# Performance work log

Hardware: AMD Instinct MI355X
Metric: run time of the kernel (lower is better)

The kernel has to match this reference:

```python
import jax, jax.numpy as jnp
import numpy as np

NUCLEIC_ACID_CUTOFF = 30.0
OTHER_CUTOFF = 15.0


def _cdist(x):
    # x: [b, n, 3] -> pairwise euclidean distances [b, n, n]
    sq = jnp.sum(x * x, axis=-1)  # [b, n]
    d2 = sq[:, :, None] + sq[:, None, :] - 2.0 * jnp.einsum('bid,bjd->bij', x, x)
    d2 = jnp.maximum(d2, 0.0)
    # safe sqrt (zero diagonal would produce nan grads otherwise)
    safe = jnp.where(d2 > 0.0, d2, 1.0)
    return jnp.where(d2 > 0.0, jnp.sqrt(safe), 0.0)


def setup_inputs() -> dict:
    key = jax.random.key(0)
    k1, k2, k3, k4, k5 = jax.random.split(key, 5)
    b, n = 2, 4096
    # scale ~10 Angstrom spread so distances straddle the 15/30 cutoffs
    true_coords = jax.random.normal(k1, (b, n, 3), dtype=jnp.float32) * 10.0
    pred_coords = true_coords + jax.random.normal(k2, (b, n, 3), dtype=jnp.float32) * 1.5
    is_dna = jax.random.bernoulli(k3, 0.15, (b, n))
    is_rna = jax.random.bernoulli(k4, 0.15, (b, n))
    coords_mask = jax.random.bernoulli(k5, 0.95, (b, n))
    return {
        'pred_coords': pred_coords,
        'true_coords': true_coords,
        'is_dna': is_dna,
        'is_rna': is_rna,
        'coords_mask': coords_mask,
    }


def reference(pred_coords, true_coords, is_dna, is_rna, coords_mask):
    n = pred_coords.shape[1]
    pred_dists = _cdist(pred_coords)  # [b, n, n]
    true_dists = _cdist(true_coords)  # [b, n, n]
    dist_diff = jnp.abs(true_dists - pred_dists)
    eps = (
        jax.nn.sigmoid(0.5 - dist_diff)
        + jax.nn.sigmoid(1.0 - dist_diff)
        + jax.nn.sigmoid(2.0 - dist_diff)
        + jax.nn.sigmoid(4.0 - dist_diff)
    ) / 4.0

    is_nucleotide = is_dna | is_rna  # [b, n]
    is_nucleotide_pair = is_nucleotide[:, :, None] & is_nucleotide[:, None, :]
    inclusion_radius = jnp.where(
        is_nucleotide_pair,
        true_dists < NUCLEIC_ACID_CUTOFF,
        true_dists < OTHER_CUTOFF,
    )
    not_eye = ~jnp.eye(n, dtype=bool)[None, :, :]
    mask = inclusion_radius & not_eye
    mask = mask & (coords_mask[:, :, None] & coords_mask[:, None, :])

    maskf = mask.astype(eps.dtype)
    lddt_sum = jnp.sum(eps * maskf, axis=(-1, -2))  # [b]
    lddt_count = jnp.sum(maskf, axis=(-1, -2))  # [b]
    lddt = lddt_sum / jnp.maximum(lddt_count, 1.0)
    return 1.0 - jnp.mean(lddt)
```

## Files before the change

### kernel.cpp

```cpp
#include <hip/hip_runtime.h>
#include <hip/hip_bf16.h>


#define NRES 4096
#define NBATCH 2
#define TI 8

#define CUT15 21.6404256133f
#define CUT30 43.2808512267f

#define S1 66.35420923f
#define S2 678.60880385f
#define S3 2039.58217570f
#define S4 1808.04241445f
#define QP1 16.58855231f
#define QP2 339.30440193f
#define QP3 1529.68663177f
#define QP4 1808.04241445f

#define DIAG_EPS 0.80408219445f
#define LOG2E 1.44269504089f

__global__ void pack_kernel(const float* __restrict__ pred,
                            const float* __restrict__ truec,
                            const int* __restrict__ dna,
                            const int* __restrict__ rna,
                            const int* __restrict__ cm,
                            float4* __restrict__ tp,
                            float4* __restrict__ pp,
                            float* __restrict__ acc)
{
    int idx = blockIdx.x * 256 + threadIdx.x;
    if (idx >= NRES * NBATCH) return;
    float nuc = ((dna[idx] | rna[idx]) != 0) ? 1.0f : 0.0f;
    float cmf = (cm[idx] != 0) ? 1.0f : 0.0f;
    tp[idx] = make_float4(truec[3*idx+0]*LOG2E, truec[3*idx+1]*LOG2E, truec[3*idx+2]*LOG2E, nuc);
    pp[idx] = make_float4(pred[3*idx+0]*LOG2E,  pred[3*idx+1]*LOG2E,  pred[3*idx+2]*LOG2E,  cmf);

    float v = cmf;
    #pragma unroll
    for (int o = 32; o > 0; o >>= 1) v += __shfl_down(v, o, 64);
    if ((threadIdx.x & 63) == 0) atomicAdd(&acc[4 + (idx >> 12)], v);
}

__launch_bounds__(256, 4)
__global__ void lddt_main(const float4* __restrict__ tp,
                          const float4* __restrict__ pp,
                          float* __restrict__ acc)
{
    const int b    = blockIdx.y;
    const int i0   = blockIdx.x * TI;
    const int base = b * NRES;
    const int tid  = threadIdx.x;

    float tix[TI], tiy[TI], tiz[TI];
    float pix[TI], piy[TI], piz[TI];
    float cHi[TI], cLo[TI];
    #pragma unroll
    for (int r = 0; r < TI; ++r) {
        float4 t4 = tp[base + i0 + r];
        float4 p4 = pp[base + i0 + r];
        tix[r] = t4.x; tiy[r] = t4.y; tiz[r] = t4.z;
        pix[r] = p4.x; piy[r] = p4.y; piz[r] = p4.z;
        bool cmi  = (p4.w != 0.0f);
        bool nuci = (t4.w != 0.0f);
        cHi[r] = cmi ? (nuci ? CUT30 : CUT15) : -1.0f;
        cLo[r] = cmi ? CUT15 : -1.0f;
    }

    float s = 0.0f, c = 0.0f;

    float4 t4 = tp[base + tid];
    float4 p4 = pp[base + tid];

    #pragma unroll 1
    for (int jt = 0; jt < NRES / 256; ++jt) {
        const int jn = tid + (((jt + 1) & 15) << 8);
        float4 t4n = tp[base + jn];
        float4 p4n = pp[base + jn];

        const float wj   = p4.w;
        const bool  nucj = (t4.w != 0.0f);

        #pragma unroll
        for (int r = 0; r < TI; ++r) {
            float dx = tix[r] - t4.x, dy = tiy[r] - t4.y, dz = tiz[r] - t4.z;
            float dt = __builtin_amdgcn_sqrtf(dx*dx + dy*dy + dz*dz);
            float ex = pix[r] - p4.x, ey = piy[r] - p4.y, ez = piz[r] - p4.z;
            float dp = __builtin_amdgcn_sqrtf(ex*ex + ey*ey + ez*ez);

            float cutoff = nucj ? cHi[r] : cLo[r];
            float mf = (dt < cutoff) ? wj : 0.0f;

            float t = __builtin_amdgcn_exp2f(-fabsf(dt - dp));
            float Q  = 1.0f + t*(S1 + t*(S2 + t*(S3 + t*S4)));
            float Qp = QP1 + t*(QP2 + t*(QP3 + t*QP4));
            float rq = __builtin_amdgcn_rcpf(Q);

            s += mf * ((t * Qp) * rq);
            c += mf;
        }

        t4 = t4n; p4 = p4n;
    }

    #pragma unroll
    for (int o = 32; o > 0; o >>= 1) {
        s += __shfl_down(s, o, 64);
        c += __shfl_down(c, o, 64);
    }

    __shared__ float red_s[4];
    __shared__ float red_c[4];
    const int wid  = tid >> 6;
    const int lane = tid & 63;
    if (lane == 0) { red_s[wid] = s; red_c[wid] = c; }
    __syncthreads();

    if (tid == 0) {
        float ts = red_s[0] + red_s[1] + red_s[2] + red_s[3];
        float tc = red_c[0] + red_c[1] + red_c[2] + red_c[3];
        atomicAdd(&acc[b], ts);
        atomicAdd(&acc[NBATCH + b], tc);
    }
}

__global__ void lddt_final(const float* __restrict__ acc, float* __restrict__ out)
{
    float M0 = acc[4], M1 = acc[5];
    float l0 = (acc[0] - DIAG_EPS * M0) / fmaxf(acc[2] - M0, 1.0f);
    float l1 = (acc[1] - DIAG_EPS * M1) / fmaxf(acc[3] - M1, 1.0f);
    out[0] = 1.0f - 0.5f * (l0 + l1);
}

extern "C" void kernel_launch(void* const* d_in, const int* in_sizes, int n_in,
                              void* d_out, int out_size, void* d_ws, size_t ws_size,
                              hipStream_t stream) {
    const float* pred  = (const float*)d_in[0];
    const float* truec = (const float*)d_in[1];
    const int*   dna   = (const int*)d_in[2];
    const int*   rna   = (const int*)d_in[3];
    const int*   cmask = (const int*)d_in[4];
    float* out = (float*)d_out;

    char* ws = (char*)d_ws;
    float*  acc = (float*)ws;
    float4* tp  = (float4*)(ws + 1024);
    float4* pp  = (float4*)(ws + 1024 + NBATCH*NRES*16);

    (void)hipMemsetAsync(acc, 0, 8 * sizeof(float), stream);

    pack_kernel<<<(NRES*NBATCH + 255)/256, 256, 0, stream>>>(pred, truec, dna, rna, cmask, tp, pp, acc);

    dim3 grid(NRES / TI, NBATCH);
    lddt_main<<<grid, 256, 0, stream>>>(tp, pp, acc);

    lddt_final<<<1, 1, 0, stream>>>(acc, out);
}
```

Measured before the change: 54.90 us.

## Exploit pair symmetry to compute only the upper triangle of residue pairs

Splits the j dimension into 1024-wide tiles and launches a 3D grid. Blocks whose j-tile lies entirely at or below the i rows exit immediately, and straddling tiles mask out j<=i with an index compare. Because distances, cutoffs and masks are symmetric, summing only j>i halves both the numerator and the count, so the ratio is unchanged. This also removes the diagonal correction and the coords-mask count reduction. In exchange, the hot loop gains an extra compare per pair, and the grid launches many blocks that return without doing work.

```diff
diff --git a/kernel.cpp b/kernel.cpp
--- a/kernel.cpp
+++ b/kernel.cpp
@@ -5,6 +5,7 @@
 #define NRES 4096
 #define NBATCH 2
 #define TI 8
+#define JTILE 1024
 
 #define CUT15 21.6404256133f
 #define CUT30 43.2808512267f
@@ -18,7 +19,6 @@
 #define QP3 1529.68663177f
 #define QP4 1808.04241445f
 
-#define DIAG_EPS 0.80408219445f
 #define LOG2E 1.44269504089f
 
 __global__ void pack_kernel(const float* __restrict__ pred,
@@ -27,8 +27,7 @@
                             const int* __restrict__ rna,
                             const int* __restrict__ cm,
                             float4* __restrict__ tp,
-                            float4* __restrict__ pp,
-                            float* __restrict__ acc)
+                            float4* __restrict__ pp)
 {
     int idx = blockIdx.x * 256 + threadIdx.x;
     if (idx >= NRES * NBATCH) return;
@@ -36,11 +35,6 @@
     float cmf = (cm[idx] != 0) ? 1.0f : 0.0f;
     tp[idx] = make_float4(truec[3*idx+0]*LOG2E, truec[3*idx+1]*LOG2E, truec[3*idx+2]*LOG2E, nuc);
     pp[idx] = make_float4(pred[3*idx+0]*LOG2E,  pred[3*idx+1]*LOG2E,  pred[3*idx+2]*LOG2E,  cmf);
-
-    float v = cmf;
-    #pragma unroll
-    for (int o = 32; o > 0; o >>= 1) v += __shfl_down(v, o, 64);
-    if ((threadIdx.x & 63) == 0) atomicAdd(&acc[4 + (idx >> 12)], v);
 }
 
 __launch_bounds__(256, 4)
@@ -48,14 +42,20 @@
                           const float4* __restrict__ pp,
                           float* __restrict__ acc)
 {
-    const int b    = blockIdx.y;
-    const int i0   = blockIdx.x * TI;
+    const int b     = blockIdx.z;
+    const int jt    = blockIdx.y;
+    const int i0    = blockIdx.x * TI;
+    const int jbase = jt * JTILE;
+
+    if (jbase + JTILE - 1 <= i0) return;
+
     const int base = b * NRES;
     const int tid  = threadIdx.x;
+    const bool straddle = (i0 >> 10) == jt;
 
     float tix[TI], tiy[TI], tiz[TI];
     float pix[TI], piy[TI], piz[TI];
-    float cHi[TI], cLo[TI];
+    float cHi[TI], cLo[TI], jminf[TI];
     #pragma unroll
     for (int r = 0; r < TI; ++r) {
         float4 t4 = tp[base + i0 + r];
@@ -66,21 +66,23 @@
         bool nuci = (t4.w != 0.0f);
         cHi[r] = cmi ? (nuci ? CUT30 : CUT15) : -1.0f;
         cLo[r] = cmi ? CUT15 : -1.0f;
+        jminf[r] = straddle ? (float)(i0 + r) + 0.5f : -1.0f;
     }
 
     float s = 0.0f, c = 0.0f;
 
-    float4 t4 = tp[base + tid];
-    float4 p4 = pp[base + tid];
+    float4 t4 = tp[base + jbase + tid];
+    float4 p4 = pp[base + jbase + tid];
 
     #pragma unroll 1
-    for (int jt = 0; jt < NRES / 256; ++jt) {
-        const int jn = tid + (((jt + 1) & 15) << 8);
+    for (int jtl = 0; jtl < JTILE / 256; ++jtl) {
+        const int jn = jbase + tid + (((jtl + 1) & 3) << 8);
         float4 t4n = tp[base + jn];
         float4 p4n = pp[base + jn];
 
         const float wj   = p4.w;
         const bool  nucj = (t4.w != 0.0f);
+        const float fj   = (float)(jbase + tid + (jtl << 8));
 
         #pragma unroll
         for (int r = 0; r < TI; ++r) {
@@ -90,7 +92,8 @@
             float dp = __builtin_amdgcn_sqrtf(ex*ex + ey*ey + ez*ez);
 
             float cutoff = nucj ? cHi[r] : cLo[r];
-            float mf = (dt < cutoff) ? wj : 0.0f;
+            float mf = (fj > jminf[r]) ? wj : 0.0f;
+            mf = (dt < cutoff) ? mf : 0.0f;
 
             float t = __builtin_amdgcn_exp2f(-fabsf(dt - dp));
             float Q  = 1.0f + t*(S1 + t*(S2 + t*(S3 + t*S4)));
@@ -127,9 +130,8 @@
 
 __global__ void lddt_final(const float* __restrict__ acc, float* __restrict__ out)
 {
-    float M0 = acc[4], M1 = acc[5];
-    float l0 = (acc[0] - DIAG_EPS * M0) / fmaxf(acc[2] - M0, 1.0f);
-    float l1 = (acc[1] - DIAG_EPS * M1) / fmaxf(acc[3] - M1, 1.0f);
+    float l0 = acc[0] / fmaxf(acc[2], 1.0f);
+    float l1 = acc[1] / fmaxf(acc[3], 1.0f);
     out[0] = 1.0f - 0.5f * (l0 + l1);
 }
 
@@ -148,11 +150,11 @@
     float4* tp  = (float4*)(ws + 1024);
     float4* pp  = (float4*)(ws + 1024 + NBATCH*NRES*16);
 
-    (void)hipMemsetAsync(acc, 0, 8 * sizeof(float), stream);
+    (void)hipMemsetAsync(acc, 0, 4 * sizeof(float), stream);
 
-    pack_kernel<<<(NRES*NBATCH + 255)/256, 256, 0, stream>>>(pred, truec, dna, rna, cmask, tp, pp, acc);
+    pack_kernel<<<(NRES*NBATCH + 255)/256, 256, 0, stream>>>(pred, truec, dna, rna, cmask, tp, pp);
 
-    dim3 grid(NRES / TI, NBATCH);
+    dim3 grid(NRES / TI, NRES / JTILE, NBATCH);
     lddt_main<<<grid, 256, 0, stream>>>(tp, pp, acc);
 
     lddt_final<<<1, 1, 0, stream>>>(acc, out);
```

Measured after the change: 83.14 us. +51.4%, slower.

## Exploit pair symmetry to compute only half of the distance matrix

Applied to the files above, without the earlier changes.

Each row block now walks circular column offsets covering only half of the pair matrix, with edge masks to drop the diagonal and lower triangle and halve the weight of the antipodal offset. Sums and counts are both halved, so their ratio is unchanged, and the threshold in the final division is adjusted to match. This removes the diagonal-correction pass and roughly halves pair evaluations, at the cost of extra per-tile mask logic and modulo indexing.

```diff
diff --git a/kernel.cpp b/kernel.cpp
--- a/kernel.cpp
+++ b/kernel.cpp
@@ -5,6 +5,7 @@
 #define NRES 4096
 #define NBATCH 2
 #define TI 8
+#define NTILE 9
 
 #define CUT15 21.6404256133f
 #define CUT30 43.2808512267f
@@ -18,7 +19,6 @@
 #define QP3 1529.68663177f
 #define QP4 1808.04241445f
 
-#define DIAG_EPS 0.80408219445f
 #define LOG2E 1.44269504089f
 
 __global__ void pack_kernel(const float* __restrict__ pred,
@@ -27,8 +27,7 @@
                             const int* __restrict__ rna,
                             const int* __restrict__ cm,
                             float4* __restrict__ tp,
-                            float4* __restrict__ pp,
-                            float* __restrict__ acc)
+                            float4* __restrict__ pp)
 {
     int idx = blockIdx.x * 256 + threadIdx.x;
     if (idx >= NRES * NBATCH) return;
@@ -36,12 +35,28 @@
     float cmf = (cm[idx] != 0) ? 1.0f : 0.0f;
     tp[idx] = make_float4(truec[3*idx+0]*LOG2E, truec[3*idx+1]*LOG2E, truec[3*idx+2]*LOG2E, nuc);
     pp[idx] = make_float4(pred[3*idx+0]*LOG2E,  pred[3*idx+1]*LOG2E,  pred[3*idx+2]*LOG2E,  cmf);
+}
 
-    float v = cmf;
-    #pragma unroll
-    for (int o = 32; o > 0; o >>= 1) v += __shfl_down(v, o, 64);
-    if ((threadIdx.x & 63) == 0) atomicAdd(&acc[4 + (idx >> 12)], v);
-}
+#define PAIR_LOOP(MODE)                                                     \
+    _Pragma("unroll")                                                       \
+    for (int r = 0; r < TI; ++r) {                                          \
+        float dx = tix[r] - t4.x, dy = tiy[r] - t4.y, dz = tiz[r] - t4.z;   \
+        float dt = __builtin_amdgcn_sqrtf(dx*dx + dy*dy + dz*dz);           \
+        float ex = pix[r] - p4.x, ey = piy[r] - p4.y, ez = piz[r] - p4.z;   \
+        float dp = __builtin_amdgcn_sqrtf(ex*ex + ey*ey + ez*ez);           \
+        float cutoff = nucj ? cHi[r] : cLo[r];                              \
+        float mf = (dt < cutoff) ? wj : 0.0f;                               \
+        if (MODE == 1) mf = (o >= r + 1) ? mf : 0.0f;                       \
+        if (MODE == 2) { int d = o - r;                                     \
+            mf = (d <= 2048) ? mf : 0.0f;                                   \
+            mf = (d == 2048) ? 0.5f * mf : mf; }                            \
+        float t = __builtin_amdgcn_exp2f(-fabsf(dt - dp));                  \
+        float Q  = 1.0f + t*(S1 + t*(S2 + t*(S3 + t*S4)));                  \
+        float Qp = QP1 + t*(QP2 + t*(QP3 + t*QP4));                         \
+        float rq = __builtin_amdgcn_rcpf(Q);                                \
+        s += mf * ((t * Qp) * rq);                                          \
+        c += mf;                                                            \
+    }
 
 __launch_bounds__(256, 4)
 __global__ void lddt_main(const float4* __restrict__ tp,
@@ -70,44 +85,31 @@
 
     float s = 0.0f, c = 0.0f;
 
-    float4 t4 = tp[base + tid];
-    float4 p4 = pp[base + tid];
+    float4 t4 = tp[base + ((i0 + tid) & (NRES - 1))];
+    float4 p4 = pp[base + ((i0 + tid) & (NRES - 1))];
 
     #pragma unroll 1
-    for (int jt = 0; jt < NRES / 256; ++jt) {
-        const int jn = tid + (((jt + 1) & 15) << 8);
+    for (int tl = 0; tl < NTILE; ++tl) {
+        const int on = (tl == NTILE - 1) ? tid : (tl + 1) * 256 + tid;
+        const int jn = (i0 + on) & (NRES - 1);
         float4 t4n = tp[base + jn];
         float4 p4n = pp[base + jn];
 
         const float wj   = p4.w;
         const bool  nucj = (t4.w != 0.0f);
+        const int   o    = tl * 256 + tid;
 
-        #pragma unroll
-        for (int r = 0; r < TI; ++r) {
-            float dx = tix[r] - t4.x, dy = tiy[r] - t4.y, dz = tiz[r] - t4.z;
-            float dt = __builtin_amdgcn_sqrtf(dx*dx + dy*dy + dz*dz);
-            float ex = pix[r] - p4.x, ey = piy[r] - p4.y, ez = piz[r] - p4.z;
-            float dp = __builtin_amdgcn_sqrtf(ex*ex + ey*ey + ez*ez);
-
-            float cutoff = nucj ? cHi[r] : cLo[r];
-            float mf = (dt < cutoff) ? wj : 0.0f;
-
-            float t = __builtin_amdgcn_exp2f(-fabsf(dt - dp));
-            float Q  = 1.0f + t*(S1 + t*(S2 + t*(S3 + t*S4)));
-            float Qp = QP1 + t*(QP2 + t*(QP3 + t*QP4));
-            float rq = __builtin_amdgcn_rcpf(Q);
-
-            s += mf * ((t * Qp) * rq);
-            c += mf;
-        }
+        if (tl == 0)            { PAIR_LOOP(1) }
+        else if (tl == NTILE-1) { PAIR_LOOP(2) }
+        else                    { PAIR_LOOP(0) }
 
         t4 = t4n; p4 = p4n;
     }
 
     #pragma unroll
-    for (int o = 32; o > 0; o >>= 1) {
-        s += __shfl_down(s, o, 64);
-        c += __shfl_down(c, o, 64);
+    for (int off = 32; off > 0; off >>= 1) {
+        s += __shfl_down(s, off, 64);
+        c += __shfl_down(c, off, 64);
     }
 
     __shared__ float red_s[4];
@@ -127,9 +129,8 @@
 
 __global__ void lddt_final(const float* __restrict__ acc, float* __restrict__ out)
 {
-    float M0 = acc[4], M1 = acc[5];
-    float l0 = (acc[0] - DIAG_EPS * M0) / fmaxf(acc[2] - M0, 1.0f);
-    float l1 = (acc[1] - DIAG_EPS * M1) / fmaxf(acc[3] - M1, 1.0f);
+    float l0 = acc[0] / fmaxf(acc[2], 0.5f);
+    float l1 = acc[1] / fmaxf(acc[3], 0.5f);
     out[0] = 1.0f - 0.5f * (l0 + l1);
 }
 
@@ -148,9 +149,9 @@
     float4* tp  = (float4*)(ws + 1024);
     float4* pp  = (float4*)(ws + 1024 + NBATCH*NRES*16);
 
-    (void)hipMemsetAsync(acc, 0, 8 * sizeof(float), stream);
+    (void)hipMemsetAsync(acc, 0, 4 * sizeof(float), stream);
 
-    pack_kernel<<<(NRES*NBATCH + 255)/256, 256, 0, stream>>>(pred, truec, dna, rna, cmask, tp, pp, acc);
+    pack_kernel<<<(NRES*NBATCH + 255)/256, 256, 0, stream>>>(pred, truec, dna, rna, cmask, tp, pp);
 
     dim3 grid(NRES / TI, NBATCH);
     lddt_main<<<grid, 256, 0, stream>>>(tp, pp, acc);
```

Result: faster. 46.87 us (-14.6%).

## Retile pairwise loop with shared-memory j tiles and fuse final reduction

Applied to the files above, without the earlier changes.

The pairwise loop is restructured so each thread owns one i residue, and each block stages a 128-entry j tile of packed coordinates in shared memory. This replaces the old scheme of 8 i rows per block in registers with the j loop streaming from global memory. The grid becomes 16x32x2 blocks. The separate finalize kernel is removed: a completion counter with a threadfence lets the last block compute the output, saving one launch. The trade-off is more blocks, more atomics, and LDS broadcast reads in place of register reuse of the i rows.

```diff
diff --git a/kernel.cpp b/kernel.cpp
--- a/kernel.cpp
+++ b/kernel.cpp
@@ -4,7 +4,8 @@
 
 #define NRES 4096
 #define NBATCH 2
-#define TI 8
+#define TJ 128
+#define NBLOCKS (16 * 32 * NBATCH)
 
 #define CUT15 21.6404256133f
 #define CUT30 43.2808512267f
@@ -46,68 +47,61 @@
 __launch_bounds__(256, 4)
 __global__ void lddt_main(const float4* __restrict__ tp,
                           const float4* __restrict__ pp,
-                          float* __restrict__ acc)
+                          float* __restrict__ acc,
+                          unsigned int* __restrict__ done,
+                          float* __restrict__ out)
 {
-    const int b    = blockIdx.y;
-    const int i0   = blockIdx.x * TI;
+    const int b    = blockIdx.z;
+    const int j0   = blockIdx.y * TJ;
+    const int i    = blockIdx.x * 256 + threadIdx.x;
     const int base = b * NRES;
     const int tid  = threadIdx.x;
 
-    float tix[TI], tiy[TI], tiz[TI];
-    float pix[TI], piy[TI], piz[TI];
-    float cHi[TI], cLo[TI];
-    #pragma unroll
-    for (int r = 0; r < TI; ++r) {
-        float4 t4 = tp[base + i0 + r];
-        float4 p4 = pp[base + i0 + r];
-        tix[r] = t4.x; tiy[r] = t4.y; tiz[r] = t4.z;
-        pix[r] = p4.x; piy[r] = p4.y; piz[r] = p4.z;
-        bool cmi  = (p4.w != 0.0f);
-        bool nuci = (t4.w != 0.0f);
-        cHi[r] = cmi ? (nuci ? CUT30 : CUT15) : -1.0f;
-        cLo[r] = cmi ? CUT15 : -1.0f;
-    }
+    __shared__ float4 stj[TJ];
+    __shared__ float4 spj[TJ];
+
+    if (tid < TJ) stj[tid]      = tp[base + j0 + tid];
+    else          spj[tid - TJ] = pp[base + j0 + (tid - TJ)];
+
+    const float4 ti4 = tp[base + i];
+    const float4 pi4 = pp[base + i];
+    const float tix = ti4.x, tiy = ti4.y, tiz = ti4.z;
+    const float pix = pi4.x, piy = pi4.y, piz = pi4.z;
+    const bool  cmi  = (pi4.w != 0.0f);
+    const bool  nuci = (ti4.w != 0.0f);
+    const float cHi = cmi ? (nuci ? CUT30 : CUT15) : -1.0f;
+    const float cLo = cmi ? CUT15 : -1.0f;
+
+    __syncthreads();
 
     float s = 0.0f, c = 0.0f;
 
-    float4 t4 = tp[base + tid];
-    float4 p4 = pp[base + tid];
+    #pragma unroll 4
+    for (int k = 0; k < TJ; ++k) {
+        const float4 tj = stj[k];
+        const float4 pj = spj[k];
 
-    #pragma unroll 1
-    for (int jt = 0; jt < NRES / 256; ++jt) {
-        const int jn = tid + (((jt + 1) & 15) << 8);
-        float4 t4n = tp[base + jn];
-        float4 p4n = pp[base + jn];
+        float dx = tix - tj.x, dy = tiy - tj.y, dz = tiz - tj.z;
+        float dt = __builtin_amdgcn_sqrtf(dx*dx + dy*dy + dz*dz);
+        float ex = pix - pj.x, ey = piy - pj.y, ez = piz - pj.z;
+        float dp = __builtin_amdgcn_sqrtf(ex*ex + ey*ey + ez*ez);
 
-        const float wj   = p4.w;
-        const bool  nucj = (t4.w != 0.0f);
+        float cutoff = (tj.w != 0.0f) ? cHi : cLo;
+        float mf = (dt < cutoff) ? pj.w : 0.0f;
 
-        #pragma unroll
-        for (int r = 0; r < TI; ++r) {
-            float dx = tix[r] - t4.x, dy = tiy[r] - t4.y, dz = tiz[r] - t4.z;
-            float dt = __builtin_amdgcn_sqrtf(dx*dx + dy*dy + dz*dz);
-            float ex = pix[r] - p4.x, ey = piy[r] - p4.y, ez = piz[r] - p4.z;
-            float dp = __builtin_amdgcn_sqrtf(ex*ex + ey*ey + ez*ez);
+        float t = __builtin_amdgcn_exp2f(-fabsf(dt - dp));
+        float Q  = 1.0f + t*(S1 + t*(S2 + t*(S3 + t*S4)));
+        float Qp = QP1 + t*(QP2 + t*(QP3 + t*QP4));
+        float rq = __builtin_amdgcn_rcpf(Q);
 
-            float cutoff = nucj ? cHi[r] : cLo[r];
-            float mf = (dt < cutoff) ? wj : 0.0f;
-
-            float t = __builtin_amdgcn_exp2f(-fabsf(dt - dp));
-            float Q  = 1.0f + t*(S1 + t*(S2 + t*(S3 + t*S4)));
-            float Qp = QP1 + t*(QP2 + t*(QP3 + t*QP4));
-            float rq = __builtin_amdgcn_rcpf(Q);
-
-            s += mf * ((t * Qp) * rq);
-            c += mf;
-        }
-
-        t4 = t4n; p4 = p4n;
+        s += mf * ((t * Qp) * rq);
+        c += mf;
     }
 
     #pragma unroll
-    for (int o = 32; o > 0; o >>= 1) {
-        s += __shfl_down(s, o, 64);
-        c += __shfl_down(c, o, 64);
+    for (int off = 32; off > 0; off >>= 1) {
+        s += __shfl_down(s, off, 64);
+        c += __shfl_down(c, off, 64);
     }
 
     __shared__ float red_s[4];
@@ -122,15 +116,20 @@
         float tc = red_c[0] + red_c[1] + red_c[2] + red_c[3];
         atomicAdd(&acc[b], ts);
         atomicAdd(&acc[NBATCH + b], tc);
+        __threadfence();
+        unsigned int old = atomicAdd(done, 1u);
+        if (old == NBLOCKS - 1u) {
+            float a0 = __hip_atomic_load(&acc[0], __ATOMIC_ACQUIRE, __HIP_MEMORY_SCOPE_AGENT);
+            float a1 = __hip_atomic_load(&acc[1], __ATOMIC_ACQUIRE, __HIP_MEMORY_SCOPE_AGENT);
+            float c0 = __hip_atomic_load(&acc[2], __ATOMIC_ACQUIRE, __HIP_MEMORY_SCOPE_AGENT);
+            float c1 = __hip_atomic_load(&acc[3], __ATOMIC_ACQUIRE, __HIP_MEMORY_SCOPE_AGENT);
+            float M0 = __hip_atomic_load(&acc[4], __ATOMIC_ACQUIRE, __HIP_MEMORY_SCOPE_AGENT);
+            float M1 = __hip_atomic_load(&acc[5], __ATOMIC_ACQUIRE, __HIP_MEMORY_SCOPE_AGENT);
+            float l0 = (a0 - DIAG_EPS * M0) / fmaxf(c0 - M0, 1.0f);
+            float l1 = (a1 - DIAG_EPS * M1) / fmaxf(c1 - M1, 1.0f);
+            out[0] = 1.0f - 0.5f * (l0 + l1);
+        }
     }
-}
-
-__global__ void lddt_final(const float* __restrict__ acc, float* __restrict__ out)
-{
-    float M0 = acc[4], M1 = acc[5];
-    float l0 = (acc[0] - DIAG_EPS * M0) / fmaxf(acc[2] - M0, 1.0f);
-    float l1 = (acc[1] - DIAG_EPS * M1) / fmaxf(acc[3] - M1, 1.0f);
-    out[0] = 1.0f - 0.5f * (l0 + l1);
 }
 
 extern "C" void kernel_launch(void* const* d_in, const int* in_sizes, int n_in,
@@ -144,16 +143,15 @@
     float* out = (float*)d_out;
 
     char* ws = (char*)d_ws;
-    float*  acc = (float*)ws;
-    float4* tp  = (float4*)(ws + 1024);
-    float4* pp  = (float4*)(ws + 1024 + NBATCH*NRES*16);
+    float*        acc  = (float*)ws;
+    unsigned int* done = (unsigned int*)(ws + 64);
+    float4* tp = (float4*)(ws + 1024);
+    float4* pp = (float4*)(ws + 1024 + NBATCH*NRES*16);
 
-    (void)hipMemsetAsync(acc, 0, 8 * sizeof(float), stream);
+    (void)hipMemsetAsync(ws, 0, 128, stream);
 
     pack_kernel<<<(NRES*NBATCH + 255)/256, 256, 0, stream>>>(pred, truec, dna, rna, cmask, tp, pp, acc);
 
-    dim3 grid(NRES / TI, NBATCH);
-    lddt_main<<<grid, 256, 0, stream>>>(tp, pp, acc);
-
-    lddt_final<<<1, 1, 0, stream>>>(acc, out);
+    dim3 grid(NRES / 256, NRES / TJ, NBATCH);
+    lddt_main<<<grid, 256, 0, stream>>>(tp, pp, acc, done, out);
 }
```

Result: no change. 53.93 us (-1.8%).
